# Kernel tuning notes

Measured on AMD Instinct MI355X. Metric: run time of the kernel, lower is better.

## Reference

```python
import jax, jax.numpy as jnp
from jax import lax
import numpy as np

H, W = 4096, 4096
KH, KW = 15, 15


def setup_inputs() -> dict:
    key = jax.random.key(0)
    kx, kw = jax.random.split(key)
    X = jax.random.normal(kx, (H, W), dtype=jnp.float32)
    weight = jax.random.uniform(kw, (KH, KW), dtype=jnp.float32)
    bias = jnp.zeros((1,), dtype=jnp.float32)
    return {"X": X, "weight": weight, "bias": bias}


def reference(X, weight, bias):
    # Valid 2D cross-correlation (no kernel flip), matching corr2d.
    # lax.conv_general_dilated performs cross-correlation by default.
    out = lax.conv_general_dilated(
        X[None, None, :, :],            # NCHW: [1, 1, H, W]
        weight[None, None, :, :],       # OIHW: [1, 1, KH, KW]
        window_strides=(1, 1),
        padding="VALID",
    )
    return out[0, 0] + bias[0]          # [H-KH+1, W-KW+1]
```

## Files before the change

kernel.cpp:

```cpp
#include <hip/hip_runtime.h>

#define H_IN 4096
#define W_IN 4096
#define KH 15
#define KW 15
#define OH (H_IN - KH + 1)
#define OW (W_IN - KW + 1)

#define BM 64
#define BN 128
#define NJ (BN / 16)
#define SROWS (BM + KH - 1)
#define SCOLS 144
#define SSTR  160

#define S_ELEMS (SROWS * SSTR)

typedef __attribute__((ext_vector_type(8))) short short8;
typedef __attribute__((ext_vector_type(4))) float f32x4;

__device__ __forceinline__ ushort f2bf(float f) {
    union { float f; uint32_t u; } v; v.f = f;
    uint32_t r = (v.u + 0x7FFFu + ((v.u >> 16) & 1u)) >> 16;
    return (ushort)r;
}

__global__ __launch_bounds__(256, 2)
void conv2d_mfma_bf16(const float* __restrict__ X,
                      const float* __restrict__ Wt,
                      const float* __restrict__ Bias,
                      float* __restrict__ Out)
{
    __shared__ ushort s_u[S_ELEMS];

    const int tid = threadIdx.x;
    const int ox0 = blockIdx.x * BN;
    const int oy0 = blockIdx.y * BM;
    const int l = tid & 63;
    const int w = tid >> 6;

    for (int idx = tid; idx < KH * 64; idx += 256) {
        int kh = idx >> 6;
        int ll = idx & 63;
        int j  = ll & 15;
        int k0 = (ll >> 4) * 8;
        ushort* dst = &s_u[idx * 8];
#pragma unroll
        for (int t = 0; t < 8; ++t) {
            int kw = k0 + t - j;
            float wv = (kw >= 0 && kw < KW) ? Wt[kh * KW + kw] : 0.0f;
            dst[t] = f2bf(wv);
        }
    }
    __syncthreads();

    short8 bfr[KH];
#pragma unroll
    for (int kh = 0; kh < KH; ++kh)
        bfr[kh] = *reinterpret_cast<const short8*>(&s_u[(kh * 64 + l) * 8]);
    __syncthreads();

    const bool interior = (ox0 + SCOLS <= W_IN);
    for (int i = tid; i < SROWS * (SCOLS / 4); i += 256) {
        int r  = i / (SCOLS / 4);
        int c4 = i % (SCOLS / 4);
        int gy = oy0 + r; if (gy > H_IN - 1) gy = H_IN - 1;
        const float* rp = &X[(size_t)gy * W_IN];
        int gx = ox0 + c4 * 4;
        float4 v;
        if (interior) {
            v = *reinterpret_cast<const float4*>(&rp[gx]);
        } else {
            v.x = rp[min(gx + 0, W_IN - 1)];
            v.y = rp[min(gx + 1, W_IN - 1)];
            v.z = rp[min(gx + 2, W_IN - 1)];
            v.w = rp[min(gx + 3, W_IN - 1)];
        }
        uint2 pk;
        pk.x = (uint32_t)f2bf(v.x) | ((uint32_t)f2bf(v.y) << 16);
        pk.y = (uint32_t)f2bf(v.z) | ((uint32_t)f2bf(v.w) << 16);
        *reinterpret_cast<uint2*>(&s_u[r * SSTR + c4 * 4]) = pk;
    }
    __syncthreads();

    f32x4 acc[NJ];
#pragma unroll
    for (int j = 0; j < NJ; ++j) acc[j] = (f32x4){0.f, 0.f, 0.f, 0.f};

    const ushort* abase = &s_u[(w * 16 + (l & 15)) * SSTR + (l >> 4) * 8];

#pragma unroll
    for (int kh = 0; kh < KH; ++kh) {
        const ushort* arow = abase + kh * SSTR;
#pragma unroll
        for (int j = 0; j < NJ; ++j) {
            short8 a = *reinterpret_cast<const short8*>(arow + j * 16);
            acc[j] = __builtin_amdgcn_mfma_f32_16x16x32_bf16(a, bfr[kh], acc[j], 0, 0, 0);
        }
    }

    const float b = Bias[0];
    const int orow0 = oy0 + w * 16 + (l >> 4) * 4;
    const int ocol  = ox0 + (l & 15);
#pragma unroll
    for (int j = 0; j < NJ; ++j) {
        int oc = ocol + j * 16;
        if (oc < OW) {
#pragma unroll
            for (int r = 0; r < 4; ++r) {
                int orow = orow0 + r;
                if (orow < OH)
                    Out[(size_t)orow * OW + oc] = acc[j][r] + b;
            }
        }
    }
}

extern "C" void kernel_launch(void* const* d_in, const int* in_sizes, int n_in,
                              void* d_out, int out_size, void* d_ws, size_t ws_size,
                              hipStream_t stream)
{
    const float* X    = (const float*)d_in[0];
    const float* Wt   = (const float*)d_in[1];
    const float* Bias = (const float*)d_in[2];
    float* Out        = (float*)d_out;

    dim3 grid((OW + BN - 1) / BN,
              (OH + BM - 1) / BM);
    dim3 block(256);
    hipLaunchKernelGGL(conv2d_mfma_bf16, grid, block, 0, stream, X, Wt, Bias, Out);
}
```

Before: 51.84 us.

## Double-buffer LDS tiles across row-tiles per block with swizzled layout

Each block now processes four vertically consecutive 64x64 output tiles, prefetching the next tile's input into registers while computing MFMAs on the current LDS buffer, then writing it to the alternate buffer. The LDS layout switches to an XOR-swizzled 128-element row to avoid bank conflicts, and the tile width shrinks to 64 so occupancy rises to 4 blocks per CU. This is meant to hide global load latency and amortize weight setup, but it raises register pressure from the prefetch buffers and re-reads halo columns more often because tiles are narrower.

```diff
diff --git a/kernel.cpp b/kernel.cpp
--- a/kernel.cpp
+++ b/kernel.cpp
@@ -8,13 +8,18 @@
 #define OW (W_IN - KW + 1)
 
 #define BM 64
-#define BN 128
-#define NJ (BN / 16)
+#define BN 64
+#define NJ 4
 #define SROWS (BM + KH - 1)
-#define SCOLS 144
-#define SSTR  160
-
-#define S_ELEMS (SROWS * SSTR)
+#define SGRAN 16
+#define ROW_USH (SGRAN * 8)
+#define SCOL4 20
+#define STAGE_N (SROWS * SCOL4)
+#define STAGE_IT 7
+#define BUF_USH (SROWS * ROW_USH)
+#define NTX 64
+#define NTY 64
+#define TPB 4
 
 typedef __attribute__((ext_vector_type(8))) short short8;
 typedef __attribute__((ext_vector_type(4))) float f32x4;
@@ -25,26 +30,50 @@
     return (ushort)r;
 }
 
-__global__ __launch_bounds__(256, 2)
-void conv2d_mfma_bf16(const float* __restrict__ X,
+__global__ __launch_bounds__(256, 4)
+void conv2d_mfma_dbuf(const float* __restrict__ X,
                       const float* __restrict__ Wt,
                       const float* __restrict__ Bias,
                       float* __restrict__ Out)
 {
-    __shared__ ushort s_u[S_ELEMS];
+    __shared__ ushort s_buf[2][BUF_USH];
 
     const int tid = threadIdx.x;
-    const int ox0 = blockIdx.x * BN;
-    const int oy0 = blockIdx.y * BM;
-    const int l = tid & 63;
-    const int w = tid >> 6;
+    const int l   = tid & 63;
+    const int w   = tid >> 6;
+    const int btx  = blockIdx.x & (NTX - 1);
+    const int tyg0 = (blockIdx.x >> 6) * TPB;
+    const int ox0  = btx * BN;
+    const bool xint = (ox0 + SCOL4 * 4 <= W_IN);
+
+    float4 v[STAGE_IT];
+
+    {
+        const int oy0 = tyg0 * BM;
+#pragma unroll
+        for (int k = 0; k < STAGE_IT; ++k) {
+            int f = tid + 256 * k;
+            if (f < STAGE_N) {
+                int r = f / SCOL4, q = f % SCOL4;
+                int gy = min(oy0 + r, H_IN - 1);
+                const float* rp = X + (size_t)gy * W_IN;
+                int gx = ox0 + q * 4;
+                if (xint) {
+                    v[k] = *reinterpret_cast<const float4*>(rp + gx);
+                } else {
+                    v[k].x = rp[min(gx + 0, W_IN - 1)];
+                    v[k].y = rp[min(gx + 1, W_IN - 1)];
+                    v[k].z = rp[min(gx + 2, W_IN - 1)];
+                    v[k].w = rp[min(gx + 3, W_IN - 1)];
+                }
+            }
+        }
+    }
 
     for (int idx = tid; idx < KH * 64; idx += 256) {
-        int kh = idx >> 6;
-        int ll = idx & 63;
-        int j  = ll & 15;
-        int k0 = (ll >> 4) * 8;
-        ushort* dst = &s_u[idx * 8];
+        int kh = idx >> 6, ll = idx & 63;
+        int j = ll & 15, k0 = (ll >> 4) * 8;
+        ushort* dst = &s_buf[1][idx * 8];
 #pragma unroll
         for (int t = 0; t < 8; ++t) {
             int kw = k0 + t - j;
@@ -53,66 +82,121 @@
         }
     }
     __syncthreads();
-
     short8 bfr[KH];
 #pragma unroll
     for (int kh = 0; kh < KH; ++kh)
-        bfr[kh] = *reinterpret_cast<const short8*>(&s_u[(kh * 64 + l) * 8]);
+        bfr[kh] = *reinterpret_cast<const short8*>(&s_buf[1][(kh * 64 + l) * 8]);
     __syncthreads();
 
-    const bool interior = (ox0 + SCOLS <= W_IN);
-    for (int i = tid; i < SROWS * (SCOLS / 4); i += 256) {
-        int r  = i / (SCOLS / 4);
-        int c4 = i % (SCOLS / 4);
-        int gy = oy0 + r; if (gy > H_IN - 1) gy = H_IN - 1;
-        const float* rp = &X[(size_t)gy * W_IN];
-        int gx = ox0 + c4 * 4;
-        float4 v;
-        if (interior) {
-            v = *reinterpret_cast<const float4*>(&rp[gx]);
-        } else {
-            v.x = rp[min(gx + 0, W_IN - 1)];
-            v.y = rp[min(gx + 1, W_IN - 1)];
-            v.z = rp[min(gx + 2, W_IN - 1)];
-            v.w = rp[min(gx + 3, W_IN - 1)];
-        }
-        uint2 pk;
-        pk.x = (uint32_t)f2bf(v.x) | ((uint32_t)f2bf(v.y) << 16);
-        pk.y = (uint32_t)f2bf(v.z) | ((uint32_t)f2bf(v.w) << 16);
-        *reinterpret_cast<uint2*>(&s_u[r * SSTR + c4 * 4]) = pk;
+#pragma unroll
+    for (int k = 0; k < STAGE_IT; ++k) {
+        int f = tid + 256 * k;
+        if (f < STAGE_N) {
+            int r = f / SCOL4, q = f % SCOL4;
+            int g = q >> 1, h = q & 1;
+            uint2 pk;
+            pk.x = (uint32_t)f2bf(v[k].x) | ((uint32_t)f2bf(v[k].y) << 16);
+            pk.y = (uint32_t)f2bf(v[k].z) | ((uint32_t)f2bf(v[k].w) << 16);
+            *reinterpret_cast<uint2*>(
+                &s_buf[0][r * ROW_USH + ((g ^ (r & 7)) * 8) + h * 4]) = pk;
+        }
     }
     __syncthreads();
 
-    f32x4 acc[NJ];
-#pragma unroll
-    for (int j = 0; j < NJ; ++j) acc[j] = (f32x4){0.f, 0.f, 0.f, 0.f};
-
-    const ushort* abase = &s_u[(w * 16 + (l & 15)) * SSTR + (l >> 4) * 8];
-
-#pragma unroll
-    for (int kh = 0; kh < KH; ++kh) {
-        const ushort* arow = abase + kh * SSTR;
-#pragma unroll
-        for (int j = 0; j < NJ; ++j) {
-            short8 a = *reinterpret_cast<const short8*>(arow + j * 16);
-            acc[j] = __builtin_amdgcn_mfma_f32_16x16x32_bf16(a, bfr[kh], acc[j], 0, 0, 0);
-        }
-    }
-
+    const int c  = l >> 4;
+    const int r0 = w * 16 + (l & 15);
     const float b = Bias[0];
-    const int orow0 = oy0 + w * 16 + (l >> 4) * 4;
-    const int ocol  = ox0 + (l & 15);
-#pragma unroll
-    for (int j = 0; j < NJ; ++j) {
-        int oc = ocol + j * 16;
-        if (oc < OW) {
-#pragma unroll
-            for (int r = 0; r < 4; ++r) {
-                int orow = orow0 + r;
-                if (orow < OH)
-                    Out[(size_t)orow * OW + oc] = acc[j][r] + b;
-            }
-        }
+    int cur = 0;
+
+#pragma unroll 1
+    for (int t = 0; t < TPB; ++t) {
+        if (t + 1 < TPB) {
+            const int oy0 = (tyg0 + t + 1) * BM;
+#pragma unroll
+            for (int k = 0; k < STAGE_IT; ++k) {
+                int f = tid + 256 * k;
+                if (f < STAGE_N) {
+                    int r = f / SCOL4, q = f % SCOL4;
+                    int gy = min(oy0 + r, H_IN - 1);
+                    const float* rp = X + (size_t)gy * W_IN;
+                    int gx = ox0 + q * 4;
+                    if (xint) {
+                        v[k] = *reinterpret_cast<const float4*>(rp + gx);
+                    } else {
+                        v[k].x = rp[min(gx + 0, W_IN - 1)];
+                        v[k].y = rp[min(gx + 1, W_IN - 1)];
+                        v[k].z = rp[min(gx + 2, W_IN - 1)];
+                        v[k].w = rp[min(gx + 3, W_IN - 1)];
+                    }
+                }
+            }
+        }
+
+        f32x4 acc[NJ];
+#pragma unroll
+        for (int j = 0; j < NJ; ++j) acc[j] = (f32x4){0.f, 0.f, 0.f, 0.f};
+
+        const ushort* bufp = &s_buf[cur][0];
+#pragma unroll
+        for (int kh = 0; kh < KH; ++kh) {
+            int rr = r0 + kh;
+            const ushort* rowb = bufp + rr * ROW_USH;
+            int x7 = rr & 7;
+#pragma unroll
+            for (int j = 0; j < NJ; ++j) {
+                int g = 2 * j + c;
+                short8 a = *reinterpret_cast<const short8*>(rowb + ((g ^ x7) * 8));
+                acc[j] = __builtin_amdgcn_mfma_f32_16x16x32_bf16(a, bfr[kh], acc[j], 0, 0, 0);
+            }
+        }
+
+        if (t + 1 < TPB) {
+#pragma unroll
+            for (int k = 0; k < STAGE_IT; ++k) {
+                int f = tid + 256 * k;
+                if (f < STAGE_N) {
+                    int r = f / SCOL4, q = f % SCOL4;
+                    int g = q >> 1, h = q & 1;
+                    uint2 pk;
+                    pk.x = (uint32_t)f2bf(v[k].x) | ((uint32_t)f2bf(v[k].y) << 16);
+                    pk.y = (uint32_t)f2bf(v[k].z) | ((uint32_t)f2bf(v[k].w) << 16);
+                    *reinterpret_cast<uint2*>(
+                        &s_buf[cur ^ 1][r * ROW_USH + ((g ^ (r & 7)) * 8) + h * 4]) = pk;
+                }
+            }
+        }
+
+        {
+            const int oy0 = (tyg0 + t) * BM;
+            const int orow0 = oy0 + w * 16 + (l >> 4) * 4;
+            const int ocol  = ox0 + (l & 15);
+            const bool inter = (ox0 + BN <= OW) && (oy0 + BM <= OH);
+            if (inter) {
+#pragma unroll
+                for (int j = 0; j < NJ; ++j) {
+                    float* op = &Out[(size_t)orow0 * OW + ocol + j * 16];
+#pragma unroll
+                    for (int r = 0; r < 4; ++r)
+                        op[(size_t)r * OW] = acc[j][r] + b;
+                }
+            } else {
+#pragma unroll
+                for (int j = 0; j < NJ; ++j) {
+                    int oc = ocol + j * 16;
+                    if (oc < OW) {
+#pragma unroll
+                        for (int r = 0; r < 4; ++r) {
+                            int orow = orow0 + r;
+                            if (orow < OH)
+                                Out[(size_t)orow * OW + oc] = acc[j][r] + b;
+                        }
+                    }
+                }
+            }
+        }
+
+        __syncthreads();
+        cur ^= 1;
     }
 }
 
@@ -125,8 +209,7 @@
     const float* Bias = (const float*)d_in[2];
     float* Out        = (float*)d_out;
 
-    dim3 grid((OW + BN - 1) / BN,
-              (OH + BM - 1) / BM);
+    dim3 grid(NTX * (NTY / TPB));
     dim3 block(256);
-    hipLaunchKernelGGL(conv2d_mfma_bf16, grid, block, 0, stream, X, Wt, Bias, Out);
+    hipLaunchKernelGGL(conv2d_mfma_dbuf, grid, block, 0, stream, X, Wt, Bias, Out);
 }
```

New measurement: 192.3 us. 3.71x slower.

## Give each wave its own private tile and loop over several tiles per wave

Applied to the files above, without the earlier changes.

Restructures the conv so each wave stages its own 16x64 output tile (30 input rows x 80 cols) in a private LDS region with no block-wide barriers, and processes four vertically stacked tiles sequentially, reusing the weight fragments held in registers. The grid becomes 1D with fewer blocks and launch bounds raise occupancy to 4 blocks per CU. This removes block-level __syncthreads stalls and amortizes the weight setup, but the smaller tiles carry a larger halo overhead (30 rows loaded per 16 output rows instead of 78 per 64), so more input is re-read and converted. Loads and MFMA within a wave are still serialized with no prefetch.

```diff
diff --git a/kernel.cpp b/kernel.cpp
--- a/kernel.cpp
+++ b/kernel.cpp
@@ -7,14 +7,16 @@
 #define OH (H_IN - KH + 1)
 #define OW (W_IN - KW + 1)
 
-#define BM 64
-#define BN 128
-#define NJ (BN / 16)
-#define SROWS (BM + KH - 1)
-#define SCOLS 144
-#define SSTR  160
-
-#define S_ELEMS (SROWS * SSTR)
+#define NJ 4
+#define WROWS 16
+#define WCOLS (16 * NJ)
+#define SROWS (WROWS + KH - 1)
+#define SCH 10
+#define ROW_USH 96
+#define WAVE_USH (SROWS * ROW_USH)
+#define NTX 64
+#define NTY 256
+#define TPW 4
 
 typedef __attribute__((ext_vector_type(8))) short short8;
 typedef __attribute__((ext_vector_type(4))) float f32x4;
@@ -24,93 +26,119 @@
     uint32_t r = (v.u + 0x7FFFu + ((v.u >> 16) & 1u)) >> 16;
     return (ushort)r;
 }
+__device__ __forceinline__ uint32_t pk2(float a, float b) {
+    return (uint32_t)f2bf(a) | ((uint32_t)f2bf(b) << 16);
+}
 
-__global__ __launch_bounds__(256, 2)
-void conv2d_mfma_bf16(const float* __restrict__ X,
-                      const float* __restrict__ Wt,
-                      const float* __restrict__ Bias,
-                      float* __restrict__ Out)
+__global__ __launch_bounds__(256, 4)
+void conv2d_mfma_wavetile(const float* __restrict__ X,
+                          const float* __restrict__ Wt,
+                          const float* __restrict__ Bias,
+                          float* __restrict__ Out)
 {
-    __shared__ ushort s_u[S_ELEMS];
+    __shared__ ushort s[4 * WAVE_USH];
 
     const int tid = threadIdx.x;
-    const int ox0 = blockIdx.x * BN;
-    const int oy0 = blockIdx.y * BM;
     const int l = tid & 63;
     const int w = tid >> 6;
 
     for (int idx = tid; idx < KH * 64; idx += 256) {
-        int kh = idx >> 6;
-        int ll = idx & 63;
-        int j  = ll & 15;
-        int k0 = (ll >> 4) * 8;
-        ushort* dst = &s_u[idx * 8];
+        int kh = idx >> 6, ll = idx & 63;
+        int j = ll & 15, k0 = (ll >> 4) * 8;
+        ushort* dst = &s[idx * 8];
 #pragma unroll
-        for (int t = 0; t < 8; ++t) {
-            int kw = k0 + t - j;
-            float wv = (kw >= 0 && kw < KW) ? Wt[kh * KW + kw] : 0.0f;
-            dst[t] = f2bf(wv);
+        for (int u = 0; u < 8; ++u) {
+            int kw = k0 + u - j;
+            dst[u] = f2bf((kw >= 0 && kw < KW) ? Wt[kh * KW + kw] : 0.0f);
         }
     }
     __syncthreads();
-
     short8 bfr[KH];
 #pragma unroll
     for (int kh = 0; kh < KH; ++kh)
-        bfr[kh] = *reinterpret_cast<const short8*>(&s_u[(kh * 64 + l) * 8]);
+        bfr[kh] = *reinterpret_cast<const short8*>(&s[(kh * 64 + l) * 8]);
     __syncthreads();
 
-    const bool interior = (ox0 + SCOLS <= W_IN);
-    for (int i = tid; i < SROWS * (SCOLS / 4); i += 256) {
-        int r  = i / (SCOLS / 4);
-        int c4 = i % (SCOLS / 4);
-        int gy = oy0 + r; if (gy > H_IN - 1) gy = H_IN - 1;
-        const float* rp = &X[(size_t)gy * W_IN];
-        int gx = ox0 + c4 * 4;
-        float4 v;
-        if (interior) {
-            v = *reinterpret_cast<const float4*>(&rp[gx]);
-        } else {
-            v.x = rp[min(gx + 0, W_IN - 1)];
-            v.y = rp[min(gx + 1, W_IN - 1)];
-            v.z = rp[min(gx + 2, W_IN - 1)];
-            v.w = rp[min(gx + 3, W_IN - 1)];
-        }
-        uint2 pk;
-        pk.x = (uint32_t)f2bf(v.x) | ((uint32_t)f2bf(v.y) << 16);
-        pk.y = (uint32_t)f2bf(v.z) | ((uint32_t)f2bf(v.w) << 16);
-        *reinterpret_cast<uint2*>(&s_u[r * SSTR + c4 * 4]) = pk;
-    }
-    __syncthreads();
+    ushort* const my = &s[w * WAVE_USH];
+    const ushort* const abase = my + (l & 15) * ROW_USH + (l >> 4) * 8;
+    const float b = Bias[0];
 
-    f32x4 acc[NJ];
-#pragma unroll
-    for (int j = 0; j < NJ; ++j) acc[j] = (f32x4){0.f, 0.f, 0.f, 0.f};
+    const int gw  = blockIdx.x * 4 + w;
+    const int tx  = gw >> 6;
+    const int ty0 = (gw & 63) * TPW;
+    const int ox0 = tx * WCOLS;
+    const bool xint = (ox0 + SCH * 8 <= W_IN);
 
-    const ushort* abase = &s_u[(w * 16 + (l & 15)) * SSTR + (l >> 4) * 8];
+#pragma unroll 1
+    for (int t = 0; t < TPW; ++t) {
+        const int iy0 = (ty0 + t) * WROWS;
 
 #pragma unroll
-    for (int kh = 0; kh < KH; ++kh) {
-        const ushort* arow = abase + kh * SSTR;
+        for (int it = 0; it < 5; ++it) {
+            int idx = it * 64 + l;
+            if (idx < SROWS * SCH) {
+                int r = idx / SCH, q = idx % SCH;
+                int gy = min(iy0 + r, H_IN - 1);
+                const float* rp = X + (size_t)gy * W_IN;
+                int gx = ox0 + q * 8;
+                float4 va, vb;
+                if (xint) {
+                    va = *reinterpret_cast<const float4*>(rp + gx);
+                    vb = *reinterpret_cast<const float4*>(rp + gx + 4);
+                } else {
+                    va.x = rp[min(gx + 0, W_IN - 1)];
+                    va.y = rp[min(gx + 1, W_IN - 1)];
+                    va.z = rp[min(gx + 2, W_IN - 1)];
+                    va.w = rp[min(gx + 3, W_IN - 1)];
+                    vb.x = rp[min(gx + 4, W_IN - 1)];
+                    vb.y = rp[min(gx + 5, W_IN - 1)];
+                    vb.z = rp[min(gx + 6, W_IN - 1)];
+                    vb.w = rp[min(gx + 7, W_IN - 1)];
+                }
+                uint4 pk;
+                pk.x = pk2(va.x, va.y);
+                pk.y = pk2(va.z, va.w);
+                pk.z = pk2(vb.x, vb.y);
+                pk.w = pk2(vb.z, vb.w);
+                *reinterpret_cast<uint4*>(&my[r * ROW_USH + q * 8]) = pk;
+            }
+        }
+
+        f32x4 acc[NJ];
 #pragma unroll
-        for (int j = 0; j < NJ; ++j) {
-            short8 a = *reinterpret_cast<const short8*>(arow + j * 16);
-            acc[j] = __builtin_amdgcn_mfma_f32_16x16x32_bf16(a, bfr[kh], acc[j], 0, 0, 0);
+        for (int j = 0; j < NJ; ++j) acc[j] = (f32x4){0.f, 0.f, 0.f, 0.f};
+
+#pragma unroll
+        for (int kh = 0; kh < KH; ++kh) {
+#pragma unroll
+            for (int j = 0; j < NJ; ++j) {
+                short8 a = *reinterpret_cast<const short8*>(abase + kh * ROW_USH + j * 16);
+                acc[j] = __builtin_amdgcn_mfma_f32_16x16x32_bf16(a, bfr[kh], acc[j], 0, 0, 0);
+            }
         }
-    }
 
-    const float b = Bias[0];
-    const int orow0 = oy0 + w * 16 + (l >> 4) * 4;
-    const int ocol  = ox0 + (l & 15);
+        const int orow0 = iy0 + (l >> 4) * 4;
+        const int ocol  = ox0 + (l & 15);
+        if (iy0 + WROWS <= OH && ox0 + WCOLS <= OW) {
+            float* op0 = &Out[(size_t)orow0 * OW + ocol];
 #pragma unroll
-    for (int j = 0; j < NJ; ++j) {
-        int oc = ocol + j * 16;
-        if (oc < OW) {
+            for (int j = 0; j < NJ; ++j) {
 #pragma unroll
-            for (int r = 0; r < 4; ++r) {
-                int orow = orow0 + r;
-                if (orow < OH)
-                    Out[(size_t)orow * OW + oc] = acc[j][r] + b;
+                for (int r = 0; r < 4; ++r)
+                    op0[(size_t)r * OW + j * 16] = acc[j][r] + b;
+            }
+        } else {
+#pragma unroll
+            for (int j = 0; j < NJ; ++j) {
+                int oc = ocol + j * 16;
+                if (oc < OW) {
+#pragma unroll
+                    for (int r = 0; r < 4; ++r) {
+                        int orow = orow0 + r;
+                        if (orow < OH)
+                            Out[(size_t)orow * OW + oc] = acc[j][r] + b;
+                    }
+                }
             }
         }
     }
@@ -125,8 +153,7 @@
     const float* Bias = (const float*)d_in[2];
     float* Out        = (float*)d_out;
 
-    dim3 grid((OW + BN - 1) / BN,
-              (OH + BM - 1) / BM);
+    dim3 grid(NTX * NTY / (4 * TPW));
     dim3 block(256);
-    hipLaunchKernelGGL(conv2d_mfma_bf16, grid, block, 0, stream, X, Wt, Bias, Out);
+    hipLaunchKernelGGL(conv2d_mfma_wavetile, grid, block, 0, stream, X, Wt, Bias, Out);
 }
```

New measurement: 78.01 us. +50.5%, slower.
